# Kernel tuning notes

Hardware: AMD Instinct MI355X
Metric: run time of the kernel (lower is better)

## Reference

```python
import jax, jax.numpy as jnp
import numpy as np

N, H, E, C, V, K = 4096, 256, 128, 32, 64, 20


def setup_inputs() -> dict:
    key = jax.random.key(0)
    ks = jax.random.split(key, 16)
    f = lambda k, s: jax.random.normal(k, s, dtype=jnp.float32)
    return {
        "vec": f(ks[0], (N, H)),
        "inp": f(ks[1], (N, E)),
        "h_prev": f(ks[2], (N, H)),
        "c_prev": f(ks[3], (N, H)),
        "Wlin": f(ks[4], (C, V, H)) * 0.05,
        "blin": f(ks[5], (C, V)) * 0.05,
        "Wec": f(ks[6], (2, H)) * 0.05,
        "bec": f(ks[7], (2,)) * 0.05,
        "Wrel": f(ks[8], (5, H)) * 0.05,
        "brel": f(ks[9], (5,)) * 0.05,
        "W_ih": f(ks[10], (K, 4 * H, E)) * 0.05,
        "b_ih": f(ks[11], (K, 4 * H)) * 0.05,
        "W_hh": f(ks[12], (K, 4 * H, H)) * 0.05,
        "b_hh": f(ks[13], (K, 4 * H)) * 0.05,
        "category": jax.random.randint(ks[14], (N,), 0, C, dtype=jnp.int32),
        "cell_id": jax.random.randint(ks[15], (N,), 0, K, dtype=jnp.int32),
        "true_idx": jax.random.randint(jax.random.fold_in(key, 100), (N,), 0, V, dtype=jnp.int32),
        "ec_idx": jax.random.randint(jax.random.fold_in(key, 101), (N,), 0, 2, dtype=jnp.int32),
        "rel_idx": jax.random.randint(jax.random.fold_in(key, 102), (N,), 0, 5, dtype=jnp.int32),
    }


def _ce(logits, targets):
    # per-row cross entropy (same math as nn.CrossEntropyLoss per example)
    logp = jax.nn.log_softmax(logits, axis=-1)
    return -jnp.take_along_axis(logp, targets[:, None], axis=-1)[:, 0]


def reference(vec, inp, h_prev, c_prev, Wlin, blin, Wec, bec, Wrel, brel,
              W_ih, b_ih, W_hh, b_hh, category, cell_id, true_idx, ec_idx, rel_idx):
    # --- get_log_odds: per-category tiny linear head, selected by category ---
    logits_all = jnp.einsum('nh,cvh->ncv', vec, Wlin) + blin          # [N,C,V]
    logits = jnp.take_along_axis(logits_all, category[:, None, None].astype(jnp.int32), axis=1)[:, 0]  # [N,V]
    logits_ec = vec @ Wec.T + bec                                      # [N,2]
    logits_rel = vec @ Wrel.T + brel                                   # [N,5]

    # --- calculate_loss: CE over valid children + ec + rel ---
    losses = _ce(logits, true_idx) + _ce(logits_ec, ec_idx) + _ce(logits_rel, rel_idx)  # [N]

    # --- get_next: per-child-index LSTMCell, selected by cell_id ---
    gates_all = (jnp.einsum('ne,kge->nkg', inp, W_ih)
                 + jnp.einsum('nh,kgh->nkg', h_prev, W_hh)
                 + b_ih + b_hh)                                        # [N,K,4H]
    gates = jnp.take_along_axis(gates_all, cell_id[:, None, None].astype(jnp.int32), axis=1)[:, 0]  # [N,4H]
    i, f, g, o = jnp.split(gates, 4, axis=-1)                          # torch LSTMCell gate order i,f,g,o
    c_next = jax.nn.sigmoid(f) * c_prev + jax.nn.sigmoid(i) * jnp.tanh(g)
    h_next = jax.nn.sigmoid(o) * jnp.tanh(c_next)

    # pack: [N, 1 + 2H] = loss | h_next | c_next
    return jnp.concatenate([losses[:, None], h_next, c_next], axis=-1)
```

## Files before the change

### kernel.cpp

```cpp
#include <hip/hip_runtime.h>
#include <hip/hip_bf16.h>
#include <math.h>

#define Nn 4096
#define Hdim 256
#define Edim 128
#define Cdim 32
#define Vdim 64
#define Kdim 20
#define G4H 1024
#define OUTS 513

#define NB 8
#define LMAXL 64
#define MAXG (NB * LMAXL)
#define MAXT2 192
#define GRID (MAXG + MAXT2)

#define SK 512
#define SC 256
#define RK_OFF 64
#define RC_OFF (RK_OFF + Kdim * SK)

typedef short bf16x8 __attribute__((ext_vector_type(8)));
typedef float f32x4 __attribute__((ext_vector_type(4)));

__device__ __forceinline__ float sigmoidf_(float x) { return 1.0f / (1.0f + expf(-x)); }

__device__ __forceinline__ bf16x8 cvt8(float4 f0, float4 f1) {
    bf16x8 r;
    __hip_bfloat16 h;
    h = __float2bfloat16(f0.x); r[0] = *(short*)&h;
    h = __float2bfloat16(f0.y); r[1] = *(short*)&h;
    h = __float2bfloat16(f0.z); r[2] = *(short*)&h;
    h = __float2bfloat16(f0.w); r[3] = *(short*)&h;
    h = __float2bfloat16(f1.x); r[4] = *(short*)&h;
    h = __float2bfloat16(f1.y); r[5] = *(short*)&h;
    h = __float2bfloat16(f1.z); r[6] = *(short*)&h;
    h = __float2bfloat16(f1.w); r[7] = *(short*)&h;
    return r;
}

__device__ __forceinline__ void gl_lds16(const float* g, void* l) {
    __builtin_amdgcn_global_load_lds((const __attribute__((address_space(1))) void*)g,
                                     (__attribute__((address_space(3))) void*)l, 16, 0, 0);
}

__device__ __forceinline__ int swz(int r) { return ((r & 3) << 1) | ((r >> 2) & 1); }

__global__ __launch_bounds__(1024) void k_setup(const int* __restrict__ cell_id,
                                                const int* __restrict__ category,
                                                int* __restrict__ ws) {
    __shared__ int cnt[32];
    int t = threadIdx.x;
    if (t < 32) cnt[t] = 0;
    __syncthreads();
    int i0 = t * 4;
    if (blockIdx.x == 0) {
        int4 v = ((const int4*)cell_id)[t];
        int r;
        r = atomicAdd(&cnt[v.x], 1); if (r < SK) ws[RK_OFF + v.x * SK + r] = i0 + 0;
        r = atomicAdd(&cnt[v.y], 1); if (r < SK) ws[RK_OFF + v.y * SK + r] = i0 + 1;
        r = atomicAdd(&cnt[v.z], 1); if (r < SK) ws[RK_OFF + v.z * SK + r] = i0 + 2;
        r = atomicAdd(&cnt[v.w], 1); if (r < SK) ws[RK_OFF + v.w * SK + r] = i0 + 3;
        __syncthreads();
        if (t < 32) ws[t] = min(cnt[t], SK);
    } else {
        int4 v = ((const int4*)category)[t];
        int r;
        r = atomicAdd(&cnt[v.x], 1); if (r < SC) ws[RC_OFF + v.x * SC + r] = i0 + 0;
        r = atomicAdd(&cnt[v.y], 1); if (r < SC) ws[RC_OFF + v.y * SC + r] = i0 + 1;
        r = atomicAdd(&cnt[v.z], 1); if (r < SC) ws[RC_OFF + v.z * SC + r] = i0 + 2;
        r = atomicAdd(&cnt[v.w], 1); if (r < SC) ws[RC_OFF + v.w * SC + r] = i0 + 3;
        __syncthreads();
        if (t < 32) ws[32 + t] = min(cnt[t], SC);
    }
}

__global__ __launch_bounds__(256, 2) void k_main(
    const float* __restrict__ vec, const float* __restrict__ inp,
    const float* __restrict__ h_prev, const float* __restrict__ c_prev,
    const float* __restrict__ Wlin, const float* __restrict__ blin,
    const float* __restrict__ Wec, const float* __restrict__ bec,
    const float* __restrict__ Wrel, const float* __restrict__ brel,
    const float* __restrict__ W_ih, const float* __restrict__ b_ih,
    const float* __restrict__ W_hh, const float* __restrict__ b_hh,
    const int* __restrict__ true_idx, const int* __restrict__ ec_idx, const int* __restrict__ rel_idx,
    const int* __restrict__ ws,
    float* __restrict__ out)
{
    __shared__ __align__(16) char smem[81920];

    int t = threadIdx.x;
    int w = t >> 6, l = t & 63;
    int l15 = l & 15, quad = l >> 4;
    int lrow8 = l >> 3, lslot = l & 7;
    bool is_lstm = blockIdx.x < MAXG;

    int* cnt = (int*)smem;
    if (t < 32) cnt[t] = ws[(is_lstm ? 0 : 32) + t];
    __syncthreads();

    int myk, s_idx, hb0 = 0, rcount;
    if (is_lstm) {
        int b = blockIdx.x & 7, pos = blockIdx.x >> 3;
        int u = -1, sf = 0, acc = 0;
        for (int uu = b; uu < Kdim * 4; uu += NB) {
            int n = (cnt[uu >> 2] + 63) >> 6;
            if (u < 0 && pos < acc + n) { u = uu; sf = pos - acc; }
            acc += n;
        }
        if (u < 0) return;
        myk = u >> 2; hb0 = (u & 3) * 64; s_idx = sf;
        rcount = min(64, cnt[myk] - s_idx * 64);
    } else {
        int slot = blockIdx.x - MAXG;
        int u = -1, sf = 0, acc = 0;
        for (int m = 0; m < Cdim; m++) {
            int n = (cnt[m] + 31) >> 5;
            if (u < 0 && slot < acc + n) { u = m; sf = slot - acc; }
            acc += n;
        }
        if (u < 0) return;
        myk = u; s_idx = sf;
        rcount = min(32, cnt[myk] - s_idx * 32);
    }

    const int* rlist = is_lstm ? (ws + RK_OFF + myk * SK + s_idx * 64)
                               : (ws + RC_OFF + myk * SC + s_idx * 32);
    int li = is_lstm ? l : (l & 31);
    int reg_row = rlist[li < rcount ? li : rcount - 1];
    int swz_l = swz(l15);
    int p0 = (quad * 2) ^ swz_l;
    __syncthreads();

    if (is_lstm) {
        const float* Wih_k = W_ih + (size_t)myk * G4H * Edim;
        const float* Whh_k = W_hh + (size_t)myk * G4H * Hdim;

        int xr0 = w * 16 + lrow8;
        int xr1 = xr0 + 8;
        int xrow0 = __shfl(reg_row, xr0);
        int xrow1 = __shfl(reg_row, xr1);
        int xg0 = lslot ^ swz(xr0);
        int xg1 = lslot ^ swz(xr1);

        auto stageL = [&](int st, int d) {
            float* Wb = (float*)(smem + d * 40960);
            float* Xb = (float*)(smem + d * 40960 + 32768);
            int k0 = st * 32;
            const float* Wsrc; int stride, ko;
            if (k0 < Edim) { Wsrc = Wih_k; stride = Edim; ko = k0; }
            else           { Wsrc = Whh_k; stride = Hdim; ko = k0 - Edim; }
            #pragma unroll
            for (int j = 0; j < 8; j++) {
                int r = w * 64 + j * 8 + lrow8;
                int g = lslot ^ swz(r);
                int gate = r >> 6, hl = r & 63;
                gl_lds16(Wsrc + (size_t)(gate * Hdim + hb0 + hl) * stride + ko + g * 4,
                         Wb + (w * 64 + j * 8) * 32);
            }
            const float* Xs0 = (k0 < Edim) ? inp + (size_t)xrow0 * Edim + ko
                                           : h_prev + (size_t)xrow0 * Hdim + ko;
            const float* Xs1 = (k0 < Edim) ? inp + (size_t)xrow1 * Edim + ko
                                           : h_prev + (size_t)xrow1 * Hdim + ko;
            gl_lds16(Xs0 + xg0 * 4, Xb + (w * 16) * 32);
            gl_lds16(Xs1 + xg1 * 4, Xb + (w * 16 + 8) * 32);
        };

        f32x4 acc[4][4];
        #pragma unroll
        for (int m = 0; m < 4; m++)
            #pragma unroll
            for (int g = 0; g < 4; g++)
                acc[m][g] = (f32x4){0.f, 0.f, 0.f, 0.f};

        stageL(0, 0);
        for (int st = 0; st < 12; st++) {
            int cur = st & 1;
            if (st < 11) stageL(st + 1, cur ^ 1);
            if (st < 11) asm volatile("s_waitcnt vmcnt(10)" ::: "memory");
            else         asm volatile("s_waitcnt vmcnt(0)" ::: "memory");
            __builtin_amdgcn_s_barrier();
            __builtin_amdgcn_sched_barrier(0);

            float* Wb = (float*)(smem + cur * 40960);
            float* Xb = (float*)(smem + cur * 40960 + 32768);
            bf16x8 af[4], bfr[4];
            #pragma unroll
            for (int m = 0; m < 4; m++) {
                int row = m * 16 + l15;
                float4 lo = *(float4*)(Xb + row * 32 + p0 * 4);
                float4 hi = *(float4*)(Xb + row * 32 + (p0 ^ 1) * 4);
                af[m] = cvt8(lo, hi);
            }
            #pragma unroll
            for (int g = 0; g < 4; g++) {
                int row = g * 64 + w * 16 + l15;
                float4 lo = *(float4*)(Wb + row * 32 + p0 * 4);
                float4 hi = *(float4*)(Wb + row * 32 + (p0 ^ 1) * 4);
                bfr[g] = cvt8(lo, hi);
            }
            #pragma unroll
            for (int m = 0; m < 4; m++)
                #pragma unroll
                for (int g = 0; g < 4; g++)
                    acc[m][g] = __builtin_amdgcn_mfma_f32_16x16x32_bf16(af[m], bfr[g], acc[m][g], 0, 0, 0);

            __builtin_amdgcn_sched_barrier(0);
            __builtin_amdgcn_s_barrier();
        }

        int h = hb0 + w * 16 + l15;
        float bs[4];
        #pragma unroll
        for (int g = 0; g < 4; g++)
            bs[g] = b_ih[(size_t)myk * G4H + g * Hdim + h] + b_hh[(size_t)myk * G4H + g * Hdim + h];

        #pragma unroll
        for (int m = 0; m < 4; m++) {
            #pragma unroll
            for (int reg = 0; reg < 4; reg++) {
                int r = m * 16 + quad * 4 + reg;
                int row = __shfl(reg_row, r);
                if (r < rcount) {
                    float iv = acc[m][0][reg] + bs[0];
                    float fv = acc[m][1][reg] + bs[1];
                    float gv = acc[m][2][reg] + bs[2];
                    float ov = acc[m][3][reg] + bs[3];
                    float cp = c_prev[(size_t)row * Hdim + h];
                    float cn = sigmoidf_(fv) * cp + sigmoidf_(iv) * tanhf(gv);
                    float hn = sigmoidf_(ov) * tanhf(cn);
                    out[(size_t)row * OUTS + 1 + h] = hn;
                    out[(size_t)row * OUTS + 1 + Hdim + h] = cn;
                }
            }
        }
    } else {
        int m2 = myk;
        int xr = w * 8 + lrow8;
        int xrow = __shfl(reg_row, xr);
        int xg = lslot ^ swz(xr);

        auto stageS = [&](int st, int d) {
            float* Wb = (float*)(smem + d * 14336);
            float* Vb = (float*)(smem + d * 14336 + 10240);
            int ko = st * 32;
            for (int n = w; n < 10; n += 4) {
                int r = n * 8 + lrow8;
                int g = lslot ^ swz(r);
                const float* srcW;
                if (r < 64)      srcW = Wlin + ((size_t)m2 * Vdim + r) * Hdim;
                else if (r < 66) srcW = Wec + (size_t)(r - 64) * Hdim;
                else if (r < 71) srcW = Wrel + (size_t)(r - 66) * Hdim;
                else             srcW = Wlin + (size_t)m2 * Vdim * Hdim;
                gl_lds16(srcW + ko + g * 4, Wb + n * 8 * 32);
            }
            gl_lds16(vec + (size_t)xrow * Hdim + ko + xg * 4, Vb + (w * 8) * 32);
        };

        f32x4 a0[2], a1[2];
        #pragma unroll
        for (int m = 0; m < 2; m++) { a0[m] = (f32x4){0.f,0.f,0.f,0.f}; a1[m] = (f32x4){0.f,0.f,0.f,0.f}; }

        stageS(0, 0);
        for (int st = 0; st < 8; st++) {
            int cur = st & 1;
            if (st < 7) stageS(st + 1, cur ^ 1);
            if (st < 7) {
                if (w < 2) asm volatile("s_waitcnt vmcnt(4)" ::: "memory");
                else       asm volatile("s_waitcnt vmcnt(3)" ::: "memory");
            } else       asm volatile("s_waitcnt vmcnt(0)" ::: "memory");
            __builtin_amdgcn_s_barrier();
            __builtin_amdgcn_sched_barrier(0);

            float* Wb = (float*)(smem + cur * 14336);
            float* Vb = (float*)(smem + cur * 14336 + 10240);
            bf16x8 af[2];
            #pragma unroll
            for (int m = 0; m < 2; m++) {
                int row = m * 16 + l15;
                float4 lo = *(float4*)(Vb + row * 32 + p0 * 4);
                float4 hi = *(float4*)(Vb + row * 32 + (p0 ^ 1) * 4);
                af[m] = cvt8(lo, hi);
            }
            {
                int row = w * 16 + l15;
                float4 lo = *(float4*)(Wb + row * 32 + p0 * 4);
                float4 hi = *(float4*)(Wb + row * 32 + (p0 ^ 1) * 4);
                bf16x8 b0 = cvt8(lo, hi);
                a0[0] = __builtin_amdgcn_mfma_f32_16x16x32_bf16(af[0], b0, a0[0], 0, 0, 0);
                a0[1] = __builtin_amdgcn_mfma_f32_16x16x32_bf16(af[1], b0, a0[1], 0, 0, 0);
            }
            if (w == 3) {
                int row = 64 + l15;
                float4 lo = *(float4*)(Wb + row * 32 + p0 * 4);
                float4 hi = *(float4*)(Wb + row * 32 + (p0 ^ 1) * 4);
                bf16x8 b1 = cvt8(lo, hi);
                a1[0] = __builtin_amdgcn_mfma_f32_16x16x32_bf16(af[0], b1, a1[0], 0, 0, 0);
                a1[1] = __builtin_amdgcn_mfma_f32_16x16x32_bf16(af[1], b1, a1[1], 0, 0, 0);
            }
            __builtin_amdgcn_sched_barrier(0);
            __builtin_amdgcn_s_barrier();
        }

        float* Lg = (float*)(smem + 28672);
        {
            int col = w * 16 + l15;
            float bb = blin[m2 * Vdim + col];
            #pragma unroll
            for (int m = 0; m < 2; m++)
                #pragma unroll
                for (int reg = 0; reg < 4; reg++)
                    Lg[(m * 16 + quad * 4 + reg) * 84 + col] = a0[m][reg] + bb;
            if (w == 3) {
                int col1 = 64 + l15;
                float bb1 = (l15 < 2) ? bec[l15] : ((l15 < 7) ? brel[l15 - 2] : 0.f);
                #pragma unroll
                for (int m = 0; m < 2; m++)
                    #pragma unroll
                    for (int reg = 0; reg < 4; reg++)
                        Lg[(m * 16 + quad * 4 + reg) * 84 + col1] = a1[m][reg] + bb1;
            }
        }
        __syncthreads();
        for (int rr = 0; rr < 8; rr++) {
            int r = w * 8 + rr;
            if (r >= rcount) break;
            int orig = __shfl(reg_row, r);
            float lg = Lg[r * 84 + l];
            float mx = lg;
            for (int ss = 32; ss >= 1; ss >>= 1) mx = fmaxf(mx, __shfl_xor(mx, ss));
            float sm = expf(lg - mx);
            for (int ss = 32; ss >= 1; ss >>= 1) sm += __shfl_xor(sm, ss);
            float lt = __shfl(lg, true_idx[orig]);
            float loss = mx + logf(sm) - lt;
            if (l == 0) {
                float l0 = Lg[r * 84 + 64], l1 = Lg[r * 84 + 65];
                float me2 = fmaxf(l0, l1);
                loss += me2 + logf(expf(l0 - me2) + expf(l1 - me2)) - ((ec_idx[orig] == 0) ? l0 : l1);
                float rl[5] = { Lg[r * 84 + 66], Lg[r * 84 + 67], Lg[r * 84 + 68], Lg[r * 84 + 69], Lg[r * 84 + 70] };
                float mr = rl[0];
                #pragma unroll
                for (int i = 1; i < 5; i++) mr = fmaxf(mr, rl[i]);
                float sr = 0.f;
                #pragma unroll
                for (int i = 0; i < 5; i++) sr += expf(rl[i] - mr);
                loss += mr + logf(sr) - rl[rel_idx[orig]];
                out[(size_t)orig * OUTS] = loss;
            }
        }
    }
}

extern "C" void kernel_launch(void* const* d_in, const int* in_sizes, int n_in,
                              void* d_out, int out_size, void* d_ws, size_t ws_size,
                              hipStream_t stream) {
    const float* vec      = (const float*)d_in[0];
    const float* inp      = (const float*)d_in[1];
    const float* h_prev   = (const float*)d_in[2];
    const float* c_prev   = (const float*)d_in[3];
    const float* Wlin     = (const float*)d_in[4];
    const float* blin     = (const float*)d_in[5];
    const float* Wec      = (const float*)d_in[6];
    const float* bec      = (const float*)d_in[7];
    const float* Wrel     = (const float*)d_in[8];
    const float* brel     = (const float*)d_in[9];
    const float* W_ih     = (const float*)d_in[10];
    const float* b_ih     = (const float*)d_in[11];
    const float* W_hh     = (const float*)d_in[12];
    const float* b_hh     = (const float*)d_in[13];
    const int*   category = (const int*)d_in[14];
    const int*   cell_id  = (const int*)d_in[15];
    const int*   true_idx = (const int*)d_in[16];
    const int*   ec_idx   = (const int*)d_in[17];
    const int*   rel_idx  = (const int*)d_in[18];
    float* out = (float*)d_out;
    int* ws = (int*)d_ws;

    k_setup<<<2, 1024, 0, stream>>>(cell_id, category, ws);
    k_main<<<GRID, 256, 0, stream>>>(
        vec, inp, h_prev, c_prev, Wlin, blin, Wec, bec, Wrel, brel,
        W_ih, b_ih, W_hh, b_hh, true_idx, ec_idx, rel_idx, ws, out);
}
```

Measured before the change: 144.0 us.

## Pre-pack weights and activations into bf16 MFMA fragment layout in separate kernel

Adds a k_frag kernel that converts W_ih/W_hh, the loss-head weights and the gathered input rows into bf16 in the exact per-lane MFMA fragment order, stored in the workspace. The main kernel then loads fragments straight from global memory with no LDS staging, no barriers and no in-loop fp32-to-bf16 conversion. It also replaces the dynamic block-to-bucket search with a fixed grid that exits early for empty slots. The cost is an extra kernel launch and an extra round trip through global memory for the packed data, and the weights are still re-converted on every call.

```diff
diff --git a/kernel.cpp b/kernel.cpp
--- a/kernel.cpp
+++ b/kernel.cpp
@@ -11,19 +11,33 @@
 #define G4H 1024
 #define OUTS 513
 
-#define NB 8
-#define LMAXL 64
-#define MAXG (NB * LMAXL)
-#define MAXT2 192
-#define GRID (MAXG + MAXT2)
-
 #define SK 512
 #define SC 256
 #define RK_OFF 64
 #define RC_OFF (RK_OFF + Kdim * SK)
 
+#define OFF_WF 81920
+#define WF_BYTES (Kdim * 4 * 12 * 16 * 64 * 8 * 2)
+#define OFF_XF (OFF_WF + WF_BYTES)
+#define XF_BYTES (Kdim * 8 * 12 * 4 * 64 * 8 * 2)
+#define OFF_LF (OFF_XF + XF_BYTES)
+#define LF_BYTES (Cdim * 8 * 5 * 64 * 8 * 2)
+#define OFF_VF (OFF_LF + LF_BYTES)
+#define VF_BYTES (Cdim * 8 * 8 * 2 * 64 * 8 * 2)
+
+#define NWF (Kdim * 4 * 12)
+#define NXF (Kdim * 8)
+#define NLF (Cdim * 8)
+#define NVF (Cdim * 8)
+#define FRAG_GRID (NWF + NXF + NLF + NVF)
+
+#define LSTM_BLOCKS (Kdim * 8 * 4)
+#define LOSS_BLOCKS (Cdim * 8)
+#define MAIN_GRID (LSTM_BLOCKS + LOSS_BLOCKS)
+
 typedef short bf16x8 __attribute__((ext_vector_type(8)));
 typedef float f32x4 __attribute__((ext_vector_type(4)));
+typedef unsigned short u16;
 
 __device__ __forceinline__ float sigmoidf_(float x) { return 1.0f / (1.0f + expf(-x)); }
 
@@ -41,16 +55,9 @@
     return r;
 }
 
-__device__ __forceinline__ void gl_lds16(const float* g, void* l) {
-    __builtin_amdgcn_global_load_lds((const __attribute__((address_space(1))) void*)g,
-                                     (__attribute__((address_space(3))) void*)l, 16, 0, 0);
-}
-
-__device__ __forceinline__ int swz(int r) { return ((r & 3) << 1) | ((r >> 2) & 1); }
-
-__global__ __launch_bounds__(1024) void k_setup(const int* __restrict__ cell_id,
-                                                const int* __restrict__ category,
-                                                int* __restrict__ ws) {
+__global__ __launch_bounds__(1024) void k_bucket(const int* __restrict__ cell_id,
+                                                 const int* __restrict__ category,
+                                                 int* __restrict__ ws) {
     __shared__ int cnt[32];
     int t = threadIdx.x;
     if (t < 32) cnt[t] = 0;
@@ -77,96 +84,119 @@
     }
 }
 
-__global__ __launch_bounds__(256, 2) void k_main(
-    const float* __restrict__ vec, const float* __restrict__ inp,
-    const float* __restrict__ h_prev, const float* __restrict__ c_prev,
-    const float* __restrict__ Wlin, const float* __restrict__ blin,
-    const float* __restrict__ Wec, const float* __restrict__ bec,
-    const float* __restrict__ Wrel, const float* __restrict__ brel,
-    const float* __restrict__ W_ih, const float* __restrict__ b_ih,
-    const float* __restrict__ W_hh, const float* __restrict__ b_hh,
+__global__ __launch_bounds__(256) void k_frag(
+    const float* __restrict__ W_ih, const float* __restrict__ W_hh,
+    const float* __restrict__ Wlin, const float* __restrict__ Wec, const float* __restrict__ Wrel,
+    const float* __restrict__ inp, const float* __restrict__ h_prev, const float* __restrict__ vec,
+    int* __restrict__ ws)
+{
+    u16* WF = (u16*)((char*)ws + OFF_WF);
+    u16* XF = (u16*)((char*)ws + OFF_XF);
+    u16* LF = (u16*)((char*)ws + OFF_LF);
+    u16* VF = (u16*)((char*)ws + OFF_VF);
+    int b = blockIdx.x, t = threadIdx.x;
+    int l = t & 63, sub = t >> 6;
+    int c16 = l & 15, qd = l >> 4;
+
+    if (b < NWF) {
+        int k = b / 48; int r = b - k * 48; int hq = r / 12; int st = r - hq * 12;
+        int kk = st * 32 + qd * 8;
+        #pragma unroll
+        for (int rep = 0; rep < 4; rep++) {
+            int idx = sub * 4 + rep;
+            int g = idx >> 2, wv = idx & 3;
+            int row = g * Hdim + hq * 64 + wv * 16 + c16;
+            const float* p = (st < 4)
+                ? (W_ih + ((size_t)k * G4H + row) * Edim + kk)
+                : (W_hh + ((size_t)k * G4H + row) * Hdim + (kk - Edim));
+            float4 lo = *(const float4*)p;
+            float4 hi = *(const float4*)(p + 4);
+            *(bf16x8*)(WF + ((size_t)(((k * 4 + hq) * 12 + st) * 16 + idx) * 64 + l) * 8) = cvt8(lo, hi);
+        }
+    } else if (b < NWF + NXF) {
+        int b2 = b - NWF; int k = b2 >> 3; int s = b2 & 7;
+        int cntk = ws[k];
+        int rc = min(64, cntk - s * 64);
+        if (rc <= 0) return;
+        int m = sub;
+        int j = m * 16 + c16;
+        int jj = min(j, rc - 1);
+        int orig = ws[RK_OFF + k * SK + s * 64 + jj];
+        #pragma unroll
+        for (int st = 0; st < 12; st++) {
+            int kk = st * 32 + qd * 8;
+            const float* p = (st < 4) ? inp + (size_t)orig * Edim + kk
+                                      : h_prev + (size_t)orig * Hdim + (kk - Edim);
+            float4 lo = *(const float4*)p;
+            float4 hi = *(const float4*)(p + 4);
+            *(bf16x8*)(XF + ((size_t)(((k * 8 + s) * 12 + st) * 4 + m) * 64 + l) * 8) = cvt8(lo, hi);
+        }
+    } else if (b < NWF + NXF + NLF) {
+        int b3 = b - NWF - NXF; int c = b3 >> 3; int st = b3 & 7;
+        int kk = st * 32 + qd * 8;
+        for (int wg = sub; wg < 5; wg += 4) {
+            int lr = wg * 16 + c16;
+            bf16x8 v;
+            if (lr < 71) {
+                const float* p;
+                if (lr < 64)      p = Wlin + ((size_t)c * Vdim + lr) * Hdim + kk;
+                else if (lr < 66) p = Wec + (size_t)(lr - 64) * Hdim + kk;
+                else              p = Wrel + (size_t)(lr - 66) * Hdim + kk;
+                float4 lo = *(const float4*)p;
+                float4 hi = *(const float4*)(p + 4);
+                v = cvt8(lo, hi);
+            } else {
+                v = (bf16x8){0, 0, 0, 0, 0, 0, 0, 0};
+            }
+            *(bf16x8*)(LF + ((size_t)((c * 8 + st) * 5 + wg) * 64 + l) * 8) = v;
+        }
+    } else {
+        int b4 = b - NWF - NXF - NLF; int c = b4 >> 3; int s = b4 & 7;
+        int cntc = ws[32 + c];
+        int rc = min(32, cntc - s * 32);
+        if (rc <= 0) return;
+        int m = sub & 1, sh = sub >> 1;
+        int j = m * 16 + c16;
+        int jj = min(j, rc - 1);
+        int orig = ws[RC_OFF + c * SC + s * 32 + jj];
+        #pragma unroll
+        for (int q = 0; q < 4; q++) {
+            int st = sh * 4 + q;
+            int kk = st * 32 + qd * 8;
+            const float* p = vec + (size_t)orig * Hdim + kk;
+            float4 lo = *(const float4*)p;
+            float4 hi = *(const float4*)(p + 4);
+            *(bf16x8*)(VF + ((size_t)(((c * 8 + s) * 8 + st) * 2 + m) * 64 + l) * 8) = cvt8(lo, hi);
+        }
+    }
+}
+
+__global__ __launch_bounds__(256, 3) void k_main(
+    const float* __restrict__ c_prev,
+    const float* __restrict__ blin, const float* __restrict__ bec, const float* __restrict__ brel,
+    const float* __restrict__ b_ih, const float* __restrict__ b_hh,
     const int* __restrict__ true_idx, const int* __restrict__ ec_idx, const int* __restrict__ rel_idx,
     const int* __restrict__ ws,
     float* __restrict__ out)
 {
-    __shared__ __align__(16) char smem[81920];
-
-    int t = threadIdx.x;
-    int w = t >> 6, l = t & 63;
+    const u16* WF = (const u16*)((const char*)ws + OFF_WF);
+    const u16* XF = (const u16*)((const char*)ws + OFF_XF);
+    const u16* LF = (const u16*)((const char*)ws + OFF_LF);
+    const u16* VF = (const u16*)((const char*)ws + OFF_VF);
+
+    int b = blockIdx.x, t = threadIdx.x;
+    int wv = t >> 6, l = t & 63;
     int l15 = l & 15, quad = l >> 4;
-    int lrow8 = l >> 3, lslot = l & 7;
-    bool is_lstm = blockIdx.x < MAXG;
-
-    int* cnt = (int*)smem;
-    if (t < 32) cnt[t] = ws[(is_lstm ? 0 : 32) + t];
-    __syncthreads();
-
-    int myk, s_idx, hb0 = 0, rcount;
-    if (is_lstm) {
-        int b = blockIdx.x & 7, pos = blockIdx.x >> 3;
-        int u = -1, sf = 0, acc = 0;
-        for (int uu = b; uu < Kdim * 4; uu += NB) {
-            int n = (cnt[uu >> 2] + 63) >> 6;
-            if (u < 0 && pos < acc + n) { u = uu; sf = pos - acc; }
-            acc += n;
-        }
-        if (u < 0) return;
-        myk = u >> 2; hb0 = (u & 3) * 64; s_idx = sf;
-        rcount = min(64, cnt[myk] - s_idx * 64);
-    } else {
-        int slot = blockIdx.x - MAXG;
-        int u = -1, sf = 0, acc = 0;
-        for (int m = 0; m < Cdim; m++) {
-            int n = (cnt[m] + 31) >> 5;
-            if (u < 0 && slot < acc + n) { u = m; sf = slot - acc; }
-            acc += n;
-        }
-        if (u < 0) return;
-        myk = u; s_idx = sf;
-        rcount = min(32, cnt[myk] - s_idx * 32);
-    }
-
-    const int* rlist = is_lstm ? (ws + RK_OFF + myk * SK + s_idx * 64)
-                               : (ws + RC_OFF + myk * SC + s_idx * 32);
-    int li = is_lstm ? l : (l & 31);
-    int reg_row = rlist[li < rcount ? li : rcount - 1];
-    int swz_l = swz(l15);
-    int p0 = (quad * 2) ^ swz_l;
-    __syncthreads();
-
-    if (is_lstm) {
-        const float* Wih_k = W_ih + (size_t)myk * G4H * Edim;
-        const float* Whh_k = W_hh + (size_t)myk * G4H * Hdim;
-
-        int xr0 = w * 16 + lrow8;
-        int xr1 = xr0 + 8;
-        int xrow0 = __shfl(reg_row, xr0);
-        int xrow1 = __shfl(reg_row, xr1);
-        int xg0 = lslot ^ swz(xr0);
-        int xg1 = lslot ^ swz(xr1);
-
-        auto stageL = [&](int st, int d) {
-            float* Wb = (float*)(smem + d * 40960);
-            float* Xb = (float*)(smem + d * 40960 + 32768);
-            int k0 = st * 32;
-            const float* Wsrc; int stride, ko;
-            if (k0 < Edim) { Wsrc = Wih_k; stride = Edim; ko = k0; }
-            else           { Wsrc = Whh_k; stride = Hdim; ko = k0 - Edim; }
-            #pragma unroll
-            for (int j = 0; j < 8; j++) {
-                int r = w * 64 + j * 8 + lrow8;
-                int g = lslot ^ swz(r);
-                int gate = r >> 6, hl = r & 63;
-                gl_lds16(Wsrc + (size_t)(gate * Hdim + hb0 + hl) * stride + ko + g * 4,
-                         Wb + (w * 64 + j * 8) * 32);
-            }
-            const float* Xs0 = (k0 < Edim) ? inp + (size_t)xrow0 * Edim + ko
-                                           : h_prev + (size_t)xrow0 * Hdim + ko;
-            const float* Xs1 = (k0 < Edim) ? inp + (size_t)xrow1 * Edim + ko
-                                           : h_prev + (size_t)xrow1 * Hdim + ko;
-            gl_lds16(Xs0 + xg0 * 4, Xb + (w * 16) * 32);
-            gl_lds16(Xs1 + xg1 * 4, Xb + (w * 16 + 8) * 32);
-        };
+    __shared__ float Lg[32 * 84];
+
+    if (b < LSTM_BLOCKS) {
+        int k = b >> 5; int s = (b >> 2) & 7; int hq = b & 3;
+        int cntk = ws[k];
+        int rcount = min(64, cntk - s * 64);
+        if (rcount <= 0) return;
+
+        const u16* xf = XF + (size_t)((k * 8 + s) * 12) * 2048 + (size_t)l * 8;
+        const u16* wf = WF + (size_t)((k * 4 + hq) * 12) * 8192 + (size_t)(wv * 512) + (size_t)l * 8;
 
         f32x4 acc[4][4];
         #pragma unroll
@@ -175,47 +205,28 @@
             for (int g = 0; g < 4; g++)
                 acc[m][g] = (f32x4){0.f, 0.f, 0.f, 0.f};
 
-        stageL(0, 0);
         for (int st = 0; st < 12; st++) {
-            int cur = st & 1;
-            if (st < 11) stageL(st + 1, cur ^ 1);
-            if (st < 11) asm volatile("s_waitcnt vmcnt(10)" ::: "memory");
-            else         asm volatile("s_waitcnt vmcnt(0)" ::: "memory");
-            __builtin_amdgcn_s_barrier();
-            __builtin_amdgcn_sched_barrier(0);
-
-            float* Wb = (float*)(smem + cur * 40960);
-            float* Xb = (float*)(smem + cur * 40960 + 32768);
+            const u16* xs = xf + st * 2048;
+            const u16* wp = wf + st * 8192;
             bf16x8 af[4], bfr[4];
             #pragma unroll
-            for (int m = 0; m < 4; m++) {
-                int row = m * 16 + l15;
-                float4 lo = *(float4*)(Xb + row * 32 + p0 * 4);
-                float4 hi = *(float4*)(Xb + row * 32 + (p0 ^ 1) * 4);
-                af[m] = cvt8(lo, hi);
-            }
-            #pragma unroll
-            for (int g = 0; g < 4; g++) {
-                int row = g * 64 + w * 16 + l15;
-                float4 lo = *(float4*)(Wb + row * 32 + p0 * 4);
-                float4 hi = *(float4*)(Wb + row * 32 + (p0 ^ 1) * 4);
-                bfr[g] = cvt8(lo, hi);
-            }
+            for (int m = 0; m < 4; m++) af[m] = *(const bf16x8*)(xs + m * 512);
+            #pragma unroll
+            for (int g = 0; g < 4; g++) bfr[g] = *(const bf16x8*)(wp + g * 2048);
             #pragma unroll
             for (int m = 0; m < 4; m++)
                 #pragma unroll
                 for (int g = 0; g < 4; g++)
                     acc[m][g] = __builtin_amdgcn_mfma_f32_16x16x32_bf16(af[m], bfr[g], acc[m][g], 0, 0, 0);
-
-            __builtin_amdgcn_sched_barrier(0);
-            __builtin_amdgcn_s_barrier();
-        }
-
-        int h = hb0 + w * 16 + l15;
+        }
+
+        int h = hq * 64 + wv * 16 + l15;
         float bs[4];
         #pragma unroll
         for (int g = 0; g < 4; g++)
-            bs[g] = b_ih[(size_t)myk * G4H + g * Hdim + h] + b_hh[(size_t)myk * G4H + g * Hdim + h];
+            bs[g] = b_ih[(size_t)k * G4H + g * Hdim + h] + b_hh[(size_t)k * G4H + g * Hdim + h];
+
+        int reg_row = ws[RK_OFF + k * SK + s * 64 + min(l, rcount - 1)];
 
         #pragma unroll
         for (int m = 0; m < 4; m++) {
@@ -237,83 +248,42 @@
             }
         }
     } else {
-        int m2 = myk;
-        int xr = w * 8 + lrow8;
-        int xrow = __shfl(reg_row, xr);
-        int xg = lslot ^ swz(xr);
-
-        auto stageS = [&](int st, int d) {
-            float* Wb = (float*)(smem + d * 14336);
-            float* Vb = (float*)(smem + d * 14336 + 10240);
-            int ko = st * 32;
-            for (int n = w; n < 10; n += 4) {
-                int r = n * 8 + lrow8;
-                int g = lslot ^ swz(r);
-                const float* srcW;
-                if (r < 64)      srcW = Wlin + ((size_t)m2 * Vdim + r) * Hdim;
-                else if (r < 66) srcW = Wec + (size_t)(r - 64) * Hdim;
-                else if (r < 71) srcW = Wrel + (size_t)(r - 66) * Hdim;
-                else             srcW = Wlin + (size_t)m2 * Vdim * Hdim;
-                gl_lds16(srcW + ko + g * 4, Wb + n * 8 * 32);
-            }
-            gl_lds16(vec + (size_t)xrow * Hdim + ko + xg * 4, Vb + (w * 8) * 32);
-        };
+        int b2 = b - LSTM_BLOCKS; int c = b2 >> 3; int s = b2 & 7;
+        int cntc = ws[32 + c];
+        int rcount = min(32, cntc - s * 32);
+        if (rcount <= 0) return;
+
+        const u16* vf = VF + (size_t)((c * 8 + s) * 8) * 1024 + (size_t)l * 8;
+        const u16* lf = LF + (size_t)(c * 8) * 2560 + (size_t)l * 8;
 
         f32x4 a0[2], a1[2];
         #pragma unroll
         for (int m = 0; m < 2; m++) { a0[m] = (f32x4){0.f,0.f,0.f,0.f}; a1[m] = (f32x4){0.f,0.f,0.f,0.f}; }
 
-        stageS(0, 0);
         for (int st = 0; st < 8; st++) {
-            int cur = st & 1;
-            if (st < 7) stageS(st + 1, cur ^ 1);
-            if (st < 7) {
-                if (w < 2) asm volatile("s_waitcnt vmcnt(4)" ::: "memory");
-                else       asm volatile("s_waitcnt vmcnt(3)" ::: "memory");
-            } else       asm volatile("s_waitcnt vmcnt(0)" ::: "memory");
-            __builtin_amdgcn_s_barrier();
-            __builtin_amdgcn_sched_barrier(0);
-
-            float* Wb = (float*)(smem + cur * 14336);
-            float* Vb = (float*)(smem + cur * 14336 + 10240);
-            bf16x8 af[2];
-            #pragma unroll
-            for (int m = 0; m < 2; m++) {
-                int row = m * 16 + l15;
-                float4 lo = *(float4*)(Vb + row * 32 + p0 * 4);
-                float4 hi = *(float4*)(Vb + row * 32 + (p0 ^ 1) * 4);
-                af[m] = cvt8(lo, hi);
-            }
-            {
-                int row = w * 16 + l15;
-                float4 lo = *(float4*)(Wb + row * 32 + p0 * 4);
-                float4 hi = *(float4*)(Wb + row * 32 + (p0 ^ 1) * 4);
-                bf16x8 b0 = cvt8(lo, hi);
-                a0[0] = __builtin_amdgcn_mfma_f32_16x16x32_bf16(af[0], b0, a0[0], 0, 0, 0);
-                a0[1] = __builtin_amdgcn_mfma_f32_16x16x32_bf16(af[1], b0, a0[1], 0, 0, 0);
-            }
-            if (w == 3) {
-                int row = 64 + l15;
-                float4 lo = *(float4*)(Wb + row * 32 + p0 * 4);
-                float4 hi = *(float4*)(Wb + row * 32 + (p0 ^ 1) * 4);
-                bf16x8 b1 = cvt8(lo, hi);
-                a1[0] = __builtin_amdgcn_mfma_f32_16x16x32_bf16(af[0], b1, a1[0], 0, 0, 0);
-                a1[1] = __builtin_amdgcn_mfma_f32_16x16x32_bf16(af[1], b1, a1[1], 0, 0, 0);
-            }
-            __builtin_amdgcn_sched_barrier(0);
-            __builtin_amdgcn_s_barrier();
-        }
-
-        float* Lg = (float*)(smem + 28672);
+            bf16x8 af0 = *(const bf16x8*)(vf + st * 1024);
+            bf16x8 af1 = *(const bf16x8*)(vf + st * 1024 + 512);
+            bf16x8 b0 = *(const bf16x8*)(lf + st * 2560 + wv * 512);
+            a0[0] = __builtin_amdgcn_mfma_f32_16x16x32_bf16(af0, b0, a0[0], 0, 0, 0);
+            a0[1] = __builtin_amdgcn_mfma_f32_16x16x32_bf16(af1, b0, a0[1], 0, 0, 0);
+            if (wv == 3) {
+                bf16x8 b1 = *(const bf16x8*)(lf + st * 2560 + 4 * 512);
+                a1[0] = __builtin_amdgcn_mfma_f32_16x16x32_bf16(af0, b1, a1[0], 0, 0, 0);
+                a1[1] = __builtin_amdgcn_mfma_f32_16x16x32_bf16(af1, b1, a1[1], 0, 0, 0);
+            }
+        }
+
+        int reg_row = ws[RC_OFF + c * SC + s * 32 + min(l & 31, rcount - 1)];
+
         {
-            int col = w * 16 + l15;
-            float bb = blin[m2 * Vdim + col];
+            int col = wv * 16 + l15;
+            float bb = blin[c * Vdim + col];
             #pragma unroll
             for (int m = 0; m < 2; m++)
                 #pragma unroll
                 for (int reg = 0; reg < 4; reg++)
                     Lg[(m * 16 + quad * 4 + reg) * 84 + col] = a0[m][reg] + bb;
-            if (w == 3) {
+            if (wv == 3) {
                 int col1 = 64 + l15;
                 float bb1 = (l15 < 2) ? bec[l15] : ((l15 < 7) ? brel[l15 - 2] : 0.f);
                 #pragma unroll
@@ -325,7 +295,7 @@
         }
         __syncthreads();
         for (int rr = 0; rr < 8; rr++) {
-            int r = w * 8 + rr;
+            int r = wv * 8 + rr;
             if (r >= rcount) break;
             int orig = __shfl(reg_row, r);
             float lg = Lg[r * 84 + l];
@@ -378,8 +348,8 @@
     float* out = (float*)d_out;
     int* ws = (int*)d_ws;
 
-    k_setup<<<2, 1024, 0, stream>>>(cell_id, category, ws);
-    k_main<<<GRID, 256, 0, stream>>>(
-        vec, inp, h_prev, c_prev, Wlin, blin, Wec, bec, Wrel, brel,
-        W_ih, b_ih, W_hh, b_hh, true_idx, ec_idx, rel_idx, ws, out);
-}
+    k_bucket<<<2, 1024, 0, stream>>>(cell_id, category, ws);
+    k_frag<<<FRAG_GRID, 256, 0, stream>>>(W_ih, W_hh, Wlin, Wec, Wrel, inp, h_prev, vec, ws);
+    k_main<<<MAIN_GRID, 256, 0, stream>>>(c_prev, blin, bec, brel, b_ih, b_hh,
+                                          true_idx, ec_idx, rel_idx, ws, out);
+}
```

New measurement: 157.0 us. 9.0% more time.

## Halve per-block row tiles, precompute work-item lists, drop double buffering for occupancy

Applied to the files above, without the earlier changes.

The bucketing kernel now writes compact work-item lists for both the LSTM and loss paths, so main-kernel blocks look up their assignment directly instead of scanning counts. LSTM tiles shrink from 64 to 32 rows and loss tiles from 32 to 16 rows. Shared memory drops from 80KB to 36KB and double buffering is removed, raising launch bounds to 4 blocks per CU. The aim is better load balance and occupancy across more, smaller blocks. The cost is that weight tiles are re-read by twice as many blocks and global-to-LDS loads no longer overlap compute.

```diff
diff --git a/kernel.cpp b/kernel.cpp
--- a/kernel.cpp
+++ b/kernel.cpp
@@ -11,16 +11,18 @@
 #define G4H 1024
 #define OUTS 513
 
-#define NB 8
-#define LMAXL 64
-#define MAXG (NB * LMAXL)
-#define MAXT2 192
-#define GRID (MAXG + MAXT2)
-
 #define SK 512
 #define SC 256
 #define RK_OFF 64
 #define RC_OFF (RK_OFF + Kdim * SK)
+#define NLI 18496
+#define NSI 18497
+#define ITL 18498
+#define ITS (ITL + 640)
+
+#define LSTM_REGION 592
+#define LOSS_REGION 320
+#define GRID (LSTM_REGION + LOSS_REGION)
 
 typedef short bf16x8 __attribute__((ext_vector_type(8)));
 typedef float f32x4 __attribute__((ext_vector_type(4)));
@@ -48,10 +50,11 @@
 
 __device__ __forceinline__ int swz(int r) { return ((r & 3) << 1) | ((r >> 2) & 1); }
 
-__global__ __launch_bounds__(1024) void k_setup(const int* __restrict__ cell_id,
-                                                const int* __restrict__ category,
-                                                int* __restrict__ ws) {
+__global__ __launch_bounds__(1024) void k_bucket(const int* __restrict__ cell_id,
+                                                 const int* __restrict__ category,
+                                                 int* __restrict__ ws) {
     __shared__ int cnt[32];
+    __shared__ int off[33];
     int t = threadIdx.x;
     if (t < 32) cnt[t] = 0;
     __syncthreads();
@@ -64,6 +67,19 @@
         r = atomicAdd(&cnt[v.z], 1); if (r < SK) ws[RK_OFF + v.z * SK + r] = i0 + 2;
         r = atomicAdd(&cnt[v.w], 1); if (r < SK) ws[RK_OFF + v.w * SK + r] = i0 + 3;
         __syncthreads();
+        if (t == 0) {
+            int a = 0;
+            for (int kk = 0; kk < Kdim; kk++) { off[kk] = a; a += (min(cnt[kk], SK) + 31) >> 5; }
+            ws[NLI] = a * 4;
+        }
+        __syncthreads();
+        if (t < Kdim) {
+            int ns = (min(cnt[t], SK) + 31) >> 5;
+            int base = off[t];
+            for (int s = 0; s < ns; s++)
+                for (int hq = 0; hq < 4; hq++)
+                    ws[ITL + (base + s) * 4 + hq] = t | (s << 8) | (hq << 16);
+        }
         if (t < 32) ws[t] = min(cnt[t], SK);
     } else {
         int4 v = ((const int4*)category)[t];
@@ -73,11 +89,23 @@
         r = atomicAdd(&cnt[v.z], 1); if (r < SC) ws[RC_OFF + v.z * SC + r] = i0 + 2;
         r = atomicAdd(&cnt[v.w], 1); if (r < SC) ws[RC_OFF + v.w * SC + r] = i0 + 3;
         __syncthreads();
+        if (t == 0) {
+            int a = 0;
+            for (int cc = 0; cc < Cdim; cc++) { off[cc] = a; a += (min(cnt[cc], SC) + 15) >> 4; }
+            ws[NSI] = a;
+        }
+        __syncthreads();
+        if (t < Cdim) {
+            int ns = (min(cnt[t], SC) + 15) >> 4;
+            int base = off[t];
+            for (int s = 0; s < ns; s++)
+                ws[ITS + base + s] = t | (s << 8);
+        }
         if (t < 32) ws[32 + t] = min(cnt[t], SC);
     }
 }
 
-__global__ __launch_bounds__(256, 2) void k_main(
+__global__ __launch_bounds__(256, 4) void k_main(
     const float* __restrict__ vec, const float* __restrict__ inp,
     const float* __restrict__ h_prev, const float* __restrict__ c_prev,
     const float* __restrict__ Wlin, const float* __restrict__ blin,
@@ -89,106 +117,77 @@
     const int* __restrict__ ws,
     float* __restrict__ out)
 {
-    __shared__ __align__(16) char smem[81920];
-
-    int t = threadIdx.x;
+    __shared__ __align__(16) char smem[36864];
+
+    int b = blockIdx.x, t = threadIdx.x;
     int w = t >> 6, l = t & 63;
     int l15 = l & 15, quad = l >> 4;
     int lrow8 = l >> 3, lslot = l & 7;
-    bool is_lstm = blockIdx.x < MAXG;
-
-    int* cnt = (int*)smem;
-    if (t < 32) cnt[t] = ws[(is_lstm ? 0 : 32) + t];
-    __syncthreads();
-
-    int myk, s_idx, hb0 = 0, rcount;
-    if (is_lstm) {
-        int b = blockIdx.x & 7, pos = blockIdx.x >> 3;
-        int u = -1, sf = 0, acc = 0;
-        for (int uu = b; uu < Kdim * 4; uu += NB) {
-            int n = (cnt[uu >> 2] + 63) >> 6;
-            if (u < 0 && pos < acc + n) { u = uu; sf = pos - acc; }
-            acc += n;
-        }
-        if (u < 0) return;
-        myk = u >> 2; hb0 = (u & 3) * 64; s_idx = sf;
-        rcount = min(64, cnt[myk] - s_idx * 64);
-    } else {
-        int slot = blockIdx.x - MAXG;
-        int u = -1, sf = 0, acc = 0;
-        for (int m = 0; m < Cdim; m++) {
-            int n = (cnt[m] + 31) >> 5;
-            if (u < 0 && slot < acc + n) { u = m; sf = slot - acc; }
-            acc += n;
-        }
-        if (u < 0) return;
-        myk = u; s_idx = sf;
-        rcount = min(32, cnt[myk] - s_idx * 32);
-    }
-
-    const int* rlist = is_lstm ? (ws + RK_OFF + myk * SK + s_idx * 64)
-                               : (ws + RC_OFF + myk * SC + s_idx * 32);
-    int li = is_lstm ? l : (l & 31);
-    int reg_row = rlist[li < rcount ? li : rcount - 1];
-    int swz_l = swz(l15);
-    int p0 = (quad * 2) ^ swz_l;
-    __syncthreads();
-
-    if (is_lstm) {
-        const float* Wih_k = W_ih + (size_t)myk * G4H * Edim;
-        const float* Whh_k = W_hh + (size_t)myk * G4H * Hdim;
-
-        int xr0 = w * 16 + lrow8;
-        int xr1 = xr0 + 8;
-        int xrow0 = __shfl(reg_row, xr0);
-        int xrow1 = __shfl(reg_row, xr1);
-        int xg0 = lslot ^ swz(xr0);
-        int xg1 = lslot ^ swz(xr1);
-
-        auto stageL = [&](int st, int d) {
-            float* Wb = (float*)(smem + d * 40960);
-            float* Xb = (float*)(smem + d * 40960 + 32768);
+    int p0 = (quad * 2) ^ swz(l15);
+
+    if (b < LSTM_REGION) {
+        if (b >= ws[NLI]) return;
+        int item = ws[ITL + b];
+        int k = item & 255, s = (item >> 8) & 255, hq = item >> 16;
+        int cntk = ws[k];
+        int rcount = min(32, cntk - s * 32);
+        int reg_row = ws[RK_OFF + k * SK + s * 32 + min(l & 31, rcount - 1)];
+
+        float* Wb = (float*)smem;
+        float* Xb = (float*)(smem + 32768);
+        const float* Wih_k = W_ih + (size_t)k * G4H * Edim;
+        const float* Whh_k = W_hh + (size_t)k * G4H * Hdim;
+
+        int xr = w * 8 + lrow8;
+        int xrow = __shfl(reg_row, xr);
+        int xg = lslot ^ swz(xr);
+
+        int h = hq * 64 + w * 16 + l15;
+        float bs[4];
+        #pragma unroll
+        for (int g = 0; g < 4; g++)
+            bs[g] = b_ih[(size_t)k * G4H + g * Hdim + h] + b_hh[(size_t)k * G4H + g * Hdim + h];
+        float cp[2][4];
+        #pragma unroll
+        for (int m = 0; m < 2; m++)
+            #pragma unroll
+            for (int reg = 0; reg < 4; reg++) {
+                int r = m * 16 + quad * 4 + reg;
+                int row = __shfl(reg_row, r);
+                cp[m][reg] = c_prev[(size_t)row * Hdim + h];
+            }
+
+        f32x4 acc[2][4];
+        #pragma unroll
+        for (int m = 0; m < 2; m++)
+            #pragma unroll
+            for (int g = 0; g < 4; g++)
+                acc[m][g] = (f32x4){0.f, 0.f, 0.f, 0.f};
+
+        for (int st = 0; st < 12; st++) {
             int k0 = st * 32;
             const float* Wsrc; int stride, ko;
             if (k0 < Edim) { Wsrc = Wih_k; stride = Edim; ko = k0; }
             else           { Wsrc = Whh_k; stride = Hdim; ko = k0 - Edim; }
+            __syncthreads();
             #pragma unroll
             for (int j = 0; j < 8; j++) {
                 int r = w * 64 + j * 8 + lrow8;
                 int g = lslot ^ swz(r);
                 int gate = r >> 6, hl = r & 63;
-                gl_lds16(Wsrc + (size_t)(gate * Hdim + hb0 + hl) * stride + ko + g * 4,
+                gl_lds16(Wsrc + (size_t)(gate * Hdim + hq * 64 + hl) * stride + ko + g * 4,
                          Wb + (w * 64 + j * 8) * 32);
             }
-            const float* Xs0 = (k0 < Edim) ? inp + (size_t)xrow0 * Edim + ko
-                                           : h_prev + (size_t)xrow0 * Hdim + ko;
-            const float* Xs1 = (k0 < Edim) ? inp + (size_t)xrow1 * Edim + ko
-                                           : h_prev + (size_t)xrow1 * Hdim + ko;
-            gl_lds16(Xs0 + xg0 * 4, Xb + (w * 16) * 32);
-            gl_lds16(Xs1 + xg1 * 4, Xb + (w * 16 + 8) * 32);
-        };
-
-        f32x4 acc[4][4];
-        #pragma unroll
-        for (int m = 0; m < 4; m++)
-            #pragma unroll
-            for (int g = 0; g < 4; g++)
-                acc[m][g] = (f32x4){0.f, 0.f, 0.f, 0.f};
-
-        stageL(0, 0);
-        for (int st = 0; st < 12; st++) {
-            int cur = st & 1;
-            if (st < 11) stageL(st + 1, cur ^ 1);
-            if (st < 11) asm volatile("s_waitcnt vmcnt(10)" ::: "memory");
-            else         asm volatile("s_waitcnt vmcnt(0)" ::: "memory");
-            __builtin_amdgcn_s_barrier();
-            __builtin_amdgcn_sched_barrier(0);
-
-            float* Wb = (float*)(smem + cur * 40960);
-            float* Xb = (float*)(smem + cur * 40960 + 32768);
-            bf16x8 af[4], bfr[4];
-            #pragma unroll
-            for (int m = 0; m < 4; m++) {
+            {
+                const float* Xs = (k0 < Edim) ? inp + (size_t)xrow * Edim + ko
+                                              : h_prev + (size_t)xrow * Hdim + ko;
+                gl_lds16(Xs + xg * 4, Xb + (w * 8) * 32);
+            }
+            __syncthreads();
+
+            bf16x8 af[2], bfr[4];
+            #pragma unroll
+            for (int m = 0; m < 2; m++) {
                 int row = m * 16 + l15;
                 float4 lo = *(float4*)(Xb + row * 32 + p0 * 4);
                 float4 hi = *(float4*)(Xb + row * 32 + (p0 ^ 1) * 4);
@@ -202,23 +201,14 @@
                 bfr[g] = cvt8(lo, hi);
             }
             #pragma unroll
-            for (int m = 0; m < 4; m++)
+            for (int m = 0; m < 2; m++)
                 #pragma unroll
                 for (int g = 0; g < 4; g++)
                     acc[m][g] = __builtin_amdgcn_mfma_f32_16x16x32_bf16(af[m], bfr[g], acc[m][g], 0, 0, 0);
-
-            __builtin_amdgcn_sched_barrier(0);
-            __builtin_amdgcn_s_barrier();
-        }
-
-        int h = hb0 + w * 16 + l15;
-        float bs[4];
+        }
+
         #pragma unroll
-        for (int g = 0; g < 4; g++)
-            bs[g] = b_ih[(size_t)myk * G4H + g * Hdim + h] + b_hh[(size_t)myk * G4H + g * Hdim + h];
-
-        #pragma unroll
-        for (int m = 0; m < 4; m++) {
+        for (int m = 0; m < 2; m++) {
             #pragma unroll
             for (int reg = 0; reg < 4; reg++) {
                 int r = m * 16 + quad * 4 + reg;
@@ -228,8 +218,7 @@
                     float fv = acc[m][1][reg] + bs[1];
                     float gv = acc[m][2][reg] + bs[2];
                     float ov = acc[m][3][reg] + bs[3];
-                    float cp = c_prev[(size_t)row * Hdim + h];
-                    float cn = sigmoidf_(fv) * cp + sigmoidf_(iv) * tanhf(gv);
+                    float cn = sigmoidf_(fv) * cp[m][reg] + sigmoidf_(iv) * tanhf(gv);
                     float hn = sigmoidf_(ov) * tanhf(cn);
                     out[(size_t)row * OUTS + 1 + h] = hn;
                     out[(size_t)row * OUTS + 1 + Hdim + h] = cn;
@@ -237,95 +226,81 @@
             }
         }
     } else {
-        int m2 = myk;
-        int xr = w * 8 + lrow8;
+        int b2 = b - LSTM_REGION;
+        if (b2 >= ws[NSI]) return;
+        int item = ws[ITS + b2];
+        int c = item & 255, s = item >> 8;
+        int cntc = ws[32 + c];
+        int rcount = min(16, cntc - s * 16);
+        int reg_row = ws[RC_OFF + c * SC + s * 16 + min(l & 15, rcount - 1)];
+
+        float* Wb = (float*)smem;
+        float* Vb = (float*)(smem + 10240);
+        float* Lg = (float*)(smem + 12288);
+
+        int xr = (w >= 2) ? ((w - 2) * 8 + lrow8) : 0;
         int xrow = __shfl(reg_row, xr);
         int xg = lslot ^ swz(xr);
 
-        auto stageS = [&](int st, int d) {
-            float* Wb = (float*)(smem + d * 14336);
-            float* Vb = (float*)(smem + d * 14336 + 10240);
+        f32x4 a0 = (f32x4){0.f, 0.f, 0.f, 0.f};
+        f32x4 a1 = (f32x4){0.f, 0.f, 0.f, 0.f};
+
+        for (int st = 0; st < 8; st++) {
             int ko = st * 32;
+            __syncthreads();
             for (int n = w; n < 10; n += 4) {
                 int r = n * 8 + lrow8;
                 int g = lslot ^ swz(r);
                 const float* srcW;
-                if (r < 64)      srcW = Wlin + ((size_t)m2 * Vdim + r) * Hdim;
+                if (r < 64)      srcW = Wlin + ((size_t)c * Vdim + r) * Hdim;
                 else if (r < 66) srcW = Wec + (size_t)(r - 64) * Hdim;
                 else if (r < 71) srcW = Wrel + (size_t)(r - 66) * Hdim;
-                else             srcW = Wlin + (size_t)m2 * Vdim * Hdim;
+                else             srcW = Wlin + (size_t)c * Vdim * Hdim;
                 gl_lds16(srcW + ko + g * 4, Wb + n * 8 * 32);
             }
-            gl_lds16(vec + (size_t)xrow * Hdim + ko + xg * 4, Vb + (w * 8) * 32);
-        };
-
-        f32x4 a0[2], a1[2];
-        #pragma unroll
-        for (int m = 0; m < 2; m++) { a0[m] = (f32x4){0.f,0.f,0.f,0.f}; a1[m] = (f32x4){0.f,0.f,0.f,0.f}; }
-
-        stageS(0, 0);
-        for (int st = 0; st < 8; st++) {
-            int cur = st & 1;
-            if (st < 7) stageS(st + 1, cur ^ 1);
-            if (st < 7) {
-                if (w < 2) asm volatile("s_waitcnt vmcnt(4)" ::: "memory");
-                else       asm volatile("s_waitcnt vmcnt(3)" ::: "memory");
-            } else       asm volatile("s_waitcnt vmcnt(0)" ::: "memory");
-            __builtin_amdgcn_s_barrier();
-            __builtin_amdgcn_sched_barrier(0);
-
-            float* Wb = (float*)(smem + cur * 14336);
-            float* Vb = (float*)(smem + cur * 14336 + 10240);
-            bf16x8 af[2];
-            #pragma unroll
-            for (int m = 0; m < 2; m++) {
-                int row = m * 16 + l15;
-                float4 lo = *(float4*)(Vb + row * 32 + p0 * 4);
-                float4 hi = *(float4*)(Vb + row * 32 + (p0 ^ 1) * 4);
-                af[m] = cvt8(lo, hi);
+            if (w >= 2)
+                gl_lds16(vec + (size_t)xrow * Hdim + ko + xg * 4, Vb + ((w - 2) * 8) * 32);
+            __syncthreads();
+
+            bf16x8 af;
+            {
+                float4 lo = *(float4*)(Vb + l15 * 32 + p0 * 4);
+                float4 hi = *(float4*)(Vb + l15 * 32 + (p0 ^ 1) * 4);
+                af = cvt8(lo, hi);
             }
             {
                 int row = w * 16 + l15;
                 float4 lo = *(float4*)(Wb + row * 32 + p0 * 4);
                 float4 hi = *(float4*)(Wb + row * 32 + (p0 ^ 1) * 4);
                 bf16x8 b0 = cvt8(lo, hi);
-                a0[0] = __builtin_amdgcn_mfma_f32_16x16x32_bf16(af[0], b0, a0[0], 0, 0, 0);
-                a0[1] = __builtin_amdgcn_mfma_f32_16x16x32_bf16(af[1], b0, a0[1], 0, 0, 0);
+                a0 = __builtin_amdgcn_mfma_f32_16x16x32_bf16(af, b0, a0, 0, 0, 0);
             }
             if (w == 3) {
                 int row = 64 + l15;
                 float4 lo = *(float4*)(Wb + row * 32 + p0 * 4);
                 float4 hi = *(float4*)(Wb + row * 32 + (p0 ^ 1) * 4);
                 bf16x8 b1 = cvt8(lo, hi);
-                a1[0] = __builtin_amdgcn_mfma_f32_16x16x32_bf16(af[0], b1, a1[0], 0, 0, 0);
-                a1[1] = __builtin_amdgcn_mfma_f32_16x16x32_bf16(af[1], b1, a1[1], 0, 0, 0);
-            }
-            __builtin_amdgcn_sched_barrier(0);
-            __builtin_amdgcn_s_barrier();
-        }
-
-        float* Lg = (float*)(smem + 28672);
+                a1 = __builtin_amdgcn_mfma_f32_16x16x32_bf16(af, b1, a1, 0, 0, 0);
+            }
+        }
+        __syncthreads();
         {
             int col = w * 16 + l15;
-            float bb = blin[m2 * Vdim + col];
-            #pragma unroll
-            for (int m = 0; m < 2; m++)
-                #pragma unroll
-                for (int reg = 0; reg < 4; reg++)
-                    Lg[(m * 16 + quad * 4 + reg) * 84 + col] = a0[m][reg] + bb;
+            float bb = blin[c * Vdim + col];
+            #pragma unroll
+            for (int reg = 0; reg < 4; reg++)
+                Lg[(quad * 4 + reg) * 84 + col] = a0[reg] + bb;
             if (w == 3) {
                 int col1 = 64 + l15;
                 float bb1 = (l15 < 2) ? bec[l15] : ((l15 < 7) ? brel[l15 - 2] : 0.f);
                 #pragma unroll
-                for (int m = 0; m < 2; m++)
-                    #pragma unroll
-                    for (int reg = 0; reg < 4; reg++)
-                        Lg[(m * 16 + quad * 4 + reg) * 84 + col1] = a1[m][reg] + bb1;
-            }
-        }
-        __syncthreads();
-        for (int rr = 0; rr < 8; rr++) {
-            int r = w * 8 + rr;
+                for (int reg = 0; reg < 4; reg++)
+                    Lg[(quad * 4 + reg) * 84 + col1] = a1[reg] + bb1;
+            }
+        }
+        __syncthreads();
+        for (int rr = 0; rr < 4; rr++) {
+            int r = w * 4 + rr;
             if (r >= rcount) break;
             int orig = __shfl(reg_row, r);
             float lg = Lg[r * 84 + l];
@@ -378,7 +353,7 @@
     float* out = (float*)d_out;
     int* ws = (int*)d_ws;
 
-    k_setup<<<2, 1024, 0, stream>>>(cell_id, category, ws);
+    k_bucket<<<2, 1024, 0, stream>>>(cell_id, category, ws);
     k_main<<<GRID, 256, 0, stream>>>(
         vec, inp, h_prev, c_prev, Wlin, blin, Wec, bec, Wrel, brel,
         W_ih, b_ih, W_hh, b_hh, true_idx, ec_idx, rel_idx, ws, out);
```

Result: faster. 140.4 us (-2.5%).
